# Kernel tuning notes

Hardware: AMD Instinct MI355X
Metric: run time of the kernel (lower is better)

The kernel has to match this reference:

```python
import jax, jax.numpy as jnp
import numpy as np

N = 50000   # nodes
E = 800000  # edges (avg degree 16)
IN, H, OUT = 128, 128, 64


def setup_inputs() -> dict:
    key = jax.random.key(0)
    ks = jax.random.split(key, 8)

    def w(k, shape):
        fan_in = shape[0]
        return (jax.random.normal(k, shape, jnp.float32) / np.float32(np.sqrt(fan_in)))

    x = jax.random.normal(ks[0], (N, IN), jnp.float32)
    edge_index = jax.random.randint(ks[1], (2, E), 0, N, jnp.int64)
    return {
        "x": x,
        "edge_index": edge_index,
        "W1": w(ks[2], (IN, H)), "b1": jnp.zeros((H,), jnp.float32),
        "W2": w(ks[3], (H, H)),  "b2": jnp.zeros((H,), jnp.float32),
        "W3": w(ks[4], (H, H)),  "b3": jnp.zeros((H,), jnp.float32),
        "Wd1": w(ks[5], (H, H)), "bd1": jnp.zeros((H,), jnp.float32),
        "Wd2": w(ks[6], (H, OUT)), "bd2": jnp.zeros((OUT,), jnp.float32),
    }


def _gcn_conv(x, src, dst, norm, W, b):
    # x: [N, Cin] -> linear transform, gather along edges, normalized scatter-add
    h = x @ W                                   # [N, Cout]
    msg = h[src] * norm[:, None]                # [E+N, Cout]
    out = jax.ops.segment_sum(msg, dst, num_segments=N)
    return out + b


def reference(x, edge_index, W1, b1, W2, b2, W3, b3, Wd1, bd1, Wd2, bd2):
    # Add self-loops (PyG GCNConv default) and compute symmetric normalization.
    loops = jnp.arange(N, dtype=edge_index.dtype)
    src = jnp.concatenate([edge_index[0], loops])   # [E+N]
    dst = jnp.concatenate([edge_index[1], loops])   # [E+N]
    deg = jax.ops.segment_sum(jnp.ones_like(dst, dtype=x.dtype), dst, num_segments=N)
    dinv = jnp.where(deg > 0, jax.lax.rsqrt(deg), jnp.zeros_like(deg))
    norm = dinv[src] * dinv[dst]                    # [E+N]

    h = jax.nn.relu(_gcn_conv(x, src, dst, norm, W1, b1))
    h = jax.nn.relu(_gcn_conv(h, src, dst, norm, W2, b2))
    h = jax.nn.relu(_gcn_conv(h, src, dst, norm, W3, b3))

    h = jax.nn.relu(h @ Wd1 + bd1)
    return jax.nn.sigmoid(h @ Wd2 + bd2)            # [N, OUT]
```

## Files before the change

### kernel.cpp

```cpp
#include <hip/hip_runtime.h>
#include <hip/hip_bf16.h>
#include <hip/hip_fp16.h>

#define N_NODES 50000
#define N_EDGES 800000
#define C_H 128
#define C_OUT 64
#define NBLK 196
#define TSTRIDE 136
#define E_PAD 950272
#define MM_BLKS 782
#define TILE_N 6250

typedef __attribute__((ext_vector_type(8))) short bf16x8;
typedef __attribute__((ext_vector_type(4))) float f32x4;

static __device__ __forceinline__ float bf_lo(unsigned int u) { return __uint_as_float(u << 16); }
static __device__ __forceinline__ float bf_hi(unsigned int u) { return __uint_as_float(u & 0xffff0000u); }
static __device__ __forceinline__ unsigned short f2bf(float f) {
    __hip_bfloat16 h = __float2bfloat16(f);
    return *(unsigned short*)&h;
}
static __device__ __forceinline__ unsigned int pack2(float a, float b) {
    return (unsigned int)f2bf(a) | ((unsigned int)f2bf(b) << 16);
}
static __device__ __forceinline__ unsigned short f2h_bits(float f) {
    union { __half h; unsigned short u; } c; c.h = __float2half_rn(f); return c.u;
}
static __device__ __forceinline__ float h_bits2f(unsigned short u) {
    union { __half h; unsigned short u; } c; c.u = u; return __half2float(c.h);
}

__global__ void prep_kernel(const int* __restrict__ src, const int* __restrict__ dst,
                            int* __restrict__ counts2,
                            int* __restrict__ rank,
                            const float* __restrict__ W1, const float* __restrict__ W2,
                            const float* __restrict__ W3, const float* __restrict__ Wd1,
                            const float* __restrict__ Wd2,
                            unsigned short* __restrict__ P1, unsigned short* __restrict__ P2,
                            unsigned short* __restrict__ P3, unsigned short* __restrict__ Pd1,
                            unsigned short* __restrict__ Pd2,
                            unsigned int* __restrict__ epay) {
    int b = blockIdx.x;
    if (b < 3125) {
        int e = b * 256 + threadIdx.x;
        int d = dst[e], s = src[e];
        int t = s / TILE_N;
        rank[e] = atomicAdd(&counts2[d * 8 + t], 1);
    } else if (b < 3413) {
        int idx = (b - 3125) * 256 + threadIdx.x;
        if (idx < 4 * 16384) {
            int which = idx >> 14;
            int r = idx & 16383;
            const float* W = (which == 0) ? W1 : (which == 1) ? W2 : (which == 2) ? W3 : Wd1;
            unsigned short* P = (which == 0) ? P1 : (which == 1) ? P2 : (which == 2) ? P3 : Pd1;
            int j = r & 7, lane = (r >> 3) & 63, t = r >> 9;
            int nb = t & 7, kb = t >> 3;
            int k = kb * 32 + ((lane >> 4) << 3) + j;
            int n = nb * 16 + (lane & 15);
            P[r] = f2bf(W[(size_t)k * 128 + n]);
        } else {
            int r = idx - 65536;
            if (r < 8192) {
                int j = r & 7, lane = (r >> 3) & 63, t = r >> 9;
                int nb = t & 3, kb = t >> 2;
                int k = kb * 32 + ((lane >> 4) << 3) + j;
                int n = nb * 16 + (lane & 15);
                Pd2[r] = f2bf(Wd2[(size_t)k * 64 + n]);
            }
        }
    } else {
        int i = (b - 3413) * 256 + threadIdx.x;
        *(uint4*)(epay + (size_t)i * 4) = make_uint4(0, 0, 0, 0);
    }
}

__global__ void __launch_bounds__(256) scan1_kernel(int* __restrict__ counts2,
                                                    int* __restrict__ eblk,
                                                    int* __restrict__ bsum,
                                                    float* __restrict__ dinv) {
    __shared__ int ws[4];
    int i = blockIdx.x * 256 + threadIdx.x;
    int deg = 0;
    if (i < N_NODES) {
        int* c = counts2 + (size_t)i * 8;
        uint4 a = *(uint4*)c;
        uint4 bq = *(uint4*)(c + 4);
        int run = 0, tv;
        tv = a.x;  a.x  = run; run += tv;
        tv = a.y;  a.y  = run; run += tv;
        tv = a.z;  a.z  = run; run += tv;
        tv = a.w;  a.w  = run; run += tv;
        tv = bq.x; bq.x = run; run += tv;
        tv = bq.y; bq.y = run; run += tv;
        tv = bq.z; bq.z = run; run += tv;
        tv = bq.w; bq.w = run; run += tv;
        deg = run;
        *(uint4*)c = a;
        *(uint4*)(c + 4) = bq;
        dinv[i] = rsqrtf((float)deg + 1.0f);
    }
    int vp = (deg + 3) & ~3;
    int lane = threadIdx.x & 63, w = threadIdx.x >> 6;
    int x = vp;
    #pragma unroll
    for (int off = 1; off < 64; off <<= 1) {
        int t = __shfl_up(x, off, 64);
        if (lane >= off) x += t;
    }
    if (lane == 63) ws[w] = x;
    __syncthreads();
    if (threadIdx.x == 0) {
        int run = 0;
        #pragma unroll
        for (int k = 0; k < 4; ++k) { int t = ws[k]; ws[k] = run; run += t; }
        bsum[blockIdx.x] = run;
    }
    __syncthreads();
    if (i < N_NODES) eblk[i] = x - vp + ws[w];
}

__global__ void __launch_bounds__(256) scanB_kernel(const int* __restrict__ eblk,
                                                    const int* __restrict__ bsum,
                                                    int* __restrict__ rowptr) {
    __shared__ int ws[4];
    __shared__ int sbo;
    int i = threadIdx.x;
    int v = (i < NBLK) ? bsum[i] : 0;
    int lane = i & 63, w = i >> 6;
    int x = v;
    #pragma unroll
    for (int off = 1; off < 64; off <<= 1) {
        int t = __shfl_up(x, off, 64);
        if (lane >= off) x += t;
    }
    if (lane == 63) ws[w] = x;
    __syncthreads();
    if (i == 0) {
        int run = 0;
        #pragma unroll
        for (int k = 0; k < 4; ++k) { int t = ws[k]; ws[k] = run; run += t; }
    }
    __syncthreads();
    int excl = x - v + ws[w];
    if (i == (int)blockIdx.x) sbo = excl;
    if (blockIdx.x == 0 && i == NBLK - 1) rowptr[N_NODES] = excl + v;
    __syncthreads();
    int g = blockIdx.x * 256 + threadIdx.x;
    if (g < N_NODES) rowptr[g] = eblk[g] + sbo;
}

__global__ void __launch_bounds__(256) fill_mm_kernel(
        const float* __restrict__ x, const unsigned short* __restrict__ P1,
        unsigned short* __restrict__ XW1,
        const int* __restrict__ src, const int* __restrict__ dst,
        const float* __restrict__ dinv,
        const int* __restrict__ rowptr, const int* __restrict__ counts2,
        const int* __restrict__ rank,
        unsigned int* __restrict__ epay) {
    int b = blockIdx.x;
    if (b < MM_BLKS) {
        const int lane = threadIdx.x & 63;
        const int wave = threadIdx.x >> 6;
        const int wid  = b * 4 + wave;
        if (wid * 16 >= N_NODES) return;
        const int node = wid * 16 + (lane & 15);
        const int quad = lane >> 4;
        f32x4 acc[8];
        #pragma unroll
        for (int nb = 0; nb < 8; ++nb) acc[nb] = (f32x4){0.f, 0.f, 0.f, 0.f};
        #pragma unroll
        for (int kb = 0; kb < 4; ++kb) {
            const float* p = x + (size_t)node * 128 + kb * 32 + quad * 8;
            float4 lo = *(const float4*)p;
            float4 hi = *(const float4*)(p + 4);
            union { bf16x8 v; unsigned int u[4]; } tmp;
            tmp.u[0] = pack2(lo.x, lo.y); tmp.u[1] = pack2(lo.z, lo.w);
            tmp.u[2] = pack2(hi.x, hi.y); tmp.u[3] = pack2(hi.z, hi.w);
            #pragma unroll
            for (int nb = 0; nb < 8; ++nb) {
                bf16x8 wf = *(const bf16x8*)(P1 + ((size_t)(kb * 8 + nb) * 64 + lane) * 8);
                acc[nb] = __builtin_amdgcn_mfma_f32_16x16x32_bf16(wf, tmp.v, acc[nb], 0, 0, 0);
            }
        }
        #pragma unroll
        for (int nb = 0; nb < 8; ++nb) {
            int ch = nb * 16 + quad * 4;
            uint2 o;
            o.x = pack2(acc[nb][0], acc[nb][1]);
            o.y = pack2(acc[nb][2], acc[nb][3]);
            *(uint2*)(XW1 + (size_t)node * C_H + ch) = o;
        }
    } else {
        int e = (b - MM_BLKS) * 256 + threadIdx.x;
        if (e < N_EDGES) {
            int d = dst[e], s = src[e];
            int t = s / TILE_N;
            int pos = rowptr[d] + counts2[d * 8 + t] + rank[e];
            float nrm = dinv[s] * dinv[d];
            epay[pos] = (unsigned int)s | ((unsigned int)f2h_bits(nrm) << 16);
        }
    }
}

__global__ void __launch_bounds__(256) gather1_kernel(
        const int* __restrict__ rowptr,
        const unsigned int* __restrict__ epay,
        const float* __restrict__ dinv,
        const unsigned short* __restrict__ hin,
        const float* __restrict__ bias,
        unsigned short* __restrict__ out) {
    int t    = blockIdx.x * 256 + threadIdx.x;
    int node = t >> 4;
    int c8   = (t & 15) << 3;

    float di = dinv[node], dii = di * di;
    uint4 raw = *(const uint4*)(hin + (size_t)node * C_H + c8);
    float a0 = bf_lo(raw.x) * dii, a1 = bf_hi(raw.x) * dii;
    float a2 = bf_lo(raw.y) * dii, a3 = bf_hi(raw.y) * dii;
    float a4 = bf_lo(raw.z) * dii, a5 = bf_hi(raw.z) * dii;
    float a6 = bf_lo(raw.w) * dii, a7 = bf_hi(raw.w) * dii;
    int beg = rowptr[node], end = rowptr[node + 1];
    int p = beg;
    for (; p + 8 <= end; p += 8) {
        uint4 ev0 = *(const uint4*)(epay + p);
        uint4 ev1 = *(const uint4*)(epay + p + 4);
        unsigned int ee[8] = {ev0.x, ev0.y, ev0.z, ev0.w, ev1.x, ev1.y, ev1.z, ev1.w};
        uint4 rv[8];
        #pragma unroll
        for (int j = 0; j < 8; ++j)
            rv[j] = *(const uint4*)(hin + (size_t)(ee[j] & 0xffffu) * C_H + c8);
        #pragma unroll
        for (int j = 0; j < 8; ++j) {
            float nm = h_bits2f((unsigned short)(ee[j] >> 16));
            a0 = fmaf(bf_lo(rv[j].x), nm, a0); a1 = fmaf(bf_hi(rv[j].x), nm, a1);
            a2 = fmaf(bf_lo(rv[j].y), nm, a2); a3 = fmaf(bf_hi(rv[j].y), nm, a3);
            a4 = fmaf(bf_lo(rv[j].z), nm, a4); a5 = fmaf(bf_hi(rv[j].z), nm, a5);
            a6 = fmaf(bf_lo(rv[j].w), nm, a6); a7 = fmaf(bf_hi(rv[j].w), nm, a7);
        }
    }
    if (p < end) {
        uint4 ev = *(const uint4*)(epay + p);
        unsigned int ee[4] = {ev.x, ev.y, ev.z, ev.w};
        uint4 rv[4];
        #pragma unroll
        for (int j = 0; j < 4; ++j)
            rv[j] = *(const uint4*)(hin + (size_t)(ee[j] & 0xffffu) * C_H + c8);
        #pragma unroll
        for (int j = 0; j < 4; ++j) {
            float nm = h_bits2f((unsigned short)(ee[j] >> 16));
            a0 = fmaf(bf_lo(rv[j].x), nm, a0); a1 = fmaf(bf_hi(rv[j].x), nm, a1);
            a2 = fmaf(bf_lo(rv[j].y), nm, a2); a3 = fmaf(bf_hi(rv[j].y), nm, a3);
            a4 = fmaf(bf_lo(rv[j].z), nm, a4); a5 = fmaf(bf_hi(rv[j].z), nm, a5);
            a6 = fmaf(bf_lo(rv[j].w), nm, a6); a7 = fmaf(bf_hi(rv[j].w), nm, a7);
        }
    }
    float4 ba = *(const float4*)(bias + c8);
    float4 bb = *(const float4*)(bias + c8 + 4);
    a0 = fmaxf(a0 + ba.x, 0.f); a1 = fmaxf(a1 + ba.y, 0.f);
    a2 = fmaxf(a2 + ba.z, 0.f); a3 = fmaxf(a3 + ba.w, 0.f);
    a4 = fmaxf(a4 + bb.x, 0.f); a5 = fmaxf(a5 + bb.y, 0.f);
    a6 = fmaxf(a6 + bb.z, 0.f); a7 = fmaxf(a7 + bb.w, 0.f);
    uint4 o;
    o.x = pack2(a0, a1); o.y = pack2(a2, a3);
    o.z = pack2(a4, a5); o.w = pack2(a6, a7);
    *(uint4*)(out + (size_t)node * C_H + c8) = o;
}

template <bool FINAL>
__global__ void __launch_bounds__(256) fused_layer_kernel(
        const int* __restrict__ rowptr,
        const unsigned int* __restrict__ epay,
        const float* __restrict__ dinv,
        const unsigned short* __restrict__ hin,
        const unsigned short* __restrict__ Wp,
        const float* __restrict__ bias,
        const unsigned short* __restrict__ Wd1p,
        const float* __restrict__ bd1,
        const unsigned short* __restrict__ Wd2p,
        const float* __restrict__ bd2,
        unsigned short* __restrict__ out_b,
        float* __restrict__ out_f) {
    __shared__ unsigned short sG[16 * TSTRIDE];
    const int t = threadIdx.x;

    {
        int nl = t >> 4, c8 = (t & 15) << 3;
        int node = blockIdx.x * 16 + nl;
        float di = dinv[node], dii = di * di;
        uint4 raw = *(const uint4*)(hin + (size_t)node * C_H + c8);
        float a0 = bf_lo(raw.x) * dii, a1 = bf_hi(raw.x) * dii;
        float a2 = bf_lo(raw.y) * dii, a3 = bf_hi(raw.y) * dii;
        float a4 = bf_lo(raw.z) * dii, a5 = bf_hi(raw.z) * dii;
        float a6 = bf_lo(raw.w) * dii, a7 = bf_hi(raw.w) * dii;
        int beg = rowptr[node], end = rowptr[node + 1];
        int p = beg;
        for (; p + 8 <= end; p += 8) {
            uint4 ev0 = *(const uint4*)(epay + p);
            uint4 ev1 = *(const uint4*)(epay + p + 4);
            unsigned int ee[8] = {ev0.x, ev0.y, ev0.z, ev0.w, ev1.x, ev1.y, ev1.z, ev1.w};
            uint4 rv[8];
            #pragma unroll
            for (int j = 0; j < 8; ++j)
                rv[j] = *(const uint4*)(hin + (size_t)(ee[j] & 0xffffu) * C_H + c8);
            #pragma unroll
            for (int j = 0; j < 8; ++j) {
                float nm = h_bits2f((unsigned short)(ee[j] >> 16));
                a0 = fmaf(bf_lo(rv[j].x), nm, a0); a1 = fmaf(bf_hi(rv[j].x), nm, a1);
                a2 = fmaf(bf_lo(rv[j].y), nm, a2); a3 = fmaf(bf_hi(rv[j].y), nm, a3);
                a4 = fmaf(bf_lo(rv[j].z), nm, a4); a5 = fmaf(bf_hi(rv[j].z), nm, a5);
                a6 = fmaf(bf_lo(rv[j].w), nm, a6); a7 = fmaf(bf_hi(rv[j].w), nm, a7);
            }
        }
        if (p < end) {
            uint4 ev = *(const uint4*)(epay + p);
            unsigned int ee[4] = {ev.x, ev.y, ev.z, ev.w};
            uint4 rv[4];
            #pragma unroll
            for (int j = 0; j < 4; ++j)
                rv[j] = *(const uint4*)(hin + (size_t)(ee[j] & 0xffffu) * C_H + c8);
            #pragma unroll
            for (int j = 0; j < 4; ++j) {
                float nm = h_bits2f((unsigned short)(ee[j] >> 16));
                a0 = fmaf(bf_lo(rv[j].x), nm, a0); a1 = fmaf(bf_hi(rv[j].x), nm, a1);
                a2 = fmaf(bf_lo(rv[j].y), nm, a2); a3 = fmaf(bf_hi(rv[j].y), nm, a3);
                a4 = fmaf(bf_lo(rv[j].z), nm, a4); a5 = fmaf(bf_hi(rv[j].z), nm, a5);
                a6 = fmaf(bf_lo(rv[j].w), nm, a6); a7 = fmaf(bf_hi(rv[j].w), nm, a7);
            }
        }
        uint4 o;
        o.x = pack2(a0, a1); o.y = pack2(a2, a3);
        o.z = pack2(a4, a5); o.w = pack2(a6, a7);
        *(uint4*)(sG + nl * TSTRIDE + c8) = o;
    }
    __syncthreads();

    const int lane = t & 63, wave = t >> 6, quad = lane >> 4, row = lane & 15;
    const int node = blockIdx.x * 16 + row;

    f32x4 acc0 = (f32x4){0.f, 0.f, 0.f, 0.f};
    f32x4 acc1 = (f32x4){0.f, 0.f, 0.f, 0.f};
    const int nb0 = 2 * wave, nb1 = 2 * wave + 1;
    #pragma unroll
    for (int kb = 0; kb < 4; ++kb) {
        bf16x8 hf = *(const bf16x8*)(sG + row * TSTRIDE + kb * 32 + quad * 8);
        bf16x8 wf0 = *(const bf16x8*)(Wp + ((size_t)(kb * 8 + nb0) * 64 + lane) * 8);
        bf16x8 wf1 = *(const bf16x8*)(Wp + ((size_t)(kb * 8 + nb1) * 64 + lane) * 8);
        acc0 = __builtin_amdgcn_mfma_f32_16x16x32_bf16(wf0, hf, acc0, 0, 0, 0);
        acc1 = __builtin_amdgcn_mfma_f32_16x16x32_bf16(wf1, hf, acc1, 0, 0, 0);
    }
    float4 ba0 = *(const float4*)(bias + nb0 * 16 + quad * 4);
    float4 ba1 = *(const float4*)(bias + nb1 * 16 + quad * 4);
    float v00 = fmaxf(acc0[0] + ba0.x, 0.f), v01 = fmaxf(acc0[1] + ba0.y, 0.f);
    float v02 = fmaxf(acc0[2] + ba0.z, 0.f), v03 = fmaxf(acc0[3] + ba0.w, 0.f);
    float v10 = fmaxf(acc1[0] + ba1.x, 0.f), v11 = fmaxf(acc1[1] + ba1.y, 0.f);
    float v12 = fmaxf(acc1[2] + ba1.z, 0.f), v13 = fmaxf(acc1[3] + ba1.w, 0.f);

    if (!FINAL) {
        uint2 o0, o1;
        o0.x = pack2(v00, v01); o0.y = pack2(v02, v03);
        o1.x = pack2(v10, v11); o1.y = pack2(v12, v13);
        *(uint2*)(out_b + (size_t)node * C_H + nb0 * 16 + quad * 4) = o0;
        *(uint2*)(out_b + (size_t)node * C_H + nb1 * 16 + quad * 4) = o1;
        return;
    }

    __syncthreads();
    {
        uint2 o0, o1;
        o0.x = pack2(v00, v01); o0.y = pack2(v02, v03);
        o1.x = pack2(v10, v11); o1.y = pack2(v12, v13);
        *(uint2*)(sG + row * TSTRIDE + nb0 * 16 + quad * 4) = o0;
        *(uint2*)(sG + row * TSTRIDE + nb1 * 16 + quad * 4) = o1;
    }
    __syncthreads();

    acc0 = (f32x4){0.f, 0.f, 0.f, 0.f};
    acc1 = (f32x4){0.f, 0.f, 0.f, 0.f};
    #pragma unroll
    for (int kb = 0; kb < 4; ++kb) {
        bf16x8 hf = *(const bf16x8*)(sG + row * TSTRIDE + kb * 32 + quad * 8);
        bf16x8 wf0 = *(const bf16x8*)(Wd1p + ((size_t)(kb * 8 + nb0) * 64 + lane) * 8);
        bf16x8 wf1 = *(const bf16x8*)(Wd1p + ((size_t)(kb * 8 + nb1) * 64 + lane) * 8);
        acc0 = __builtin_amdgcn_mfma_f32_16x16x32_bf16(wf0, hf, acc0, 0, 0, 0);
        acc1 = __builtin_amdgcn_mfma_f32_16x16x32_bf16(wf1, hf, acc1, 0, 0, 0);
    }
    ba0 = *(const float4*)(bd1 + nb0 * 16 + quad * 4);
    ba1 = *(const float4*)(bd1 + nb1 * 16 + quad * 4);
    v00 = fmaxf(acc0[0] + ba0.x, 0.f); v01 = fmaxf(acc0[1] + ba0.y, 0.f);
    v02 = fmaxf(acc0[2] + ba0.z, 0.f); v03 = fmaxf(acc0[3] + ba0.w, 0.f);
    v10 = fmaxf(acc1[0] + ba1.x, 0.f); v11 = fmaxf(acc1[1] + ba1.y, 0.f);
    v12 = fmaxf(acc1[2] + ba1.z, 0.f); v13 = fmaxf(acc1[3] + ba1.w, 0.f);
    __syncthreads();
    {
        uint2 o0, o1;
        o0.x = pack2(v00, v01); o0.y = pack2(v02, v03);
        o1.x = pack2(v10, v11); o1.y = pack2(v12, v13);
        *(uint2*)(sG + row * TSTRIDE + nb0 * 16 + quad * 4) = o0;
        *(uint2*)(sG + row * TSTRIDE + nb1 * 16 + quad * 4) = o1;
    }
    __syncthreads();

    f32x4 acc = (f32x4){0.f, 0.f, 0.f, 0.f};
    #pragma unroll
    for (int kb = 0; kb < 4; ++kb) {
        bf16x8 hf = *(const bf16x8*)(sG + row * TSTRIDE + kb * 32 + quad * 8);
        bf16x8 wf = *(const bf16x8*)(Wd2p + ((size_t)(kb * 4 + wave) * 64 + lane) * 8);
        acc = __builtin_amdgcn_mfma_f32_16x16x32_bf16(wf, hf, acc, 0, 0, 0);
    }
    int ch = wave * 16 + quad * 4;
    float4 b4 = *(const float4*)(bd2 + ch);
    float4 r;
    r.x = 1.f / (1.f + expf(-(acc[0] + b4.x)));
    r.y = 1.f / (1.f + expf(-(acc[1] + b4.y)));
    r.z = 1.f / (1.f + expf(-(acc[2] + b4.z)));
    r.w = 1.f / (1.f + expf(-(acc[3] + b4.w)));
    *(float4*)(out_f + (size_t)node * C_OUT + ch) = r;
}

extern "C" void kernel_launch(void* const* d_in, const int* in_sizes, int n_in,
                              void* d_out, int out_size, void* d_ws, size_t ws_size,
                              hipStream_t stream) {
    const float* x   = (const float*)d_in[0];
    const int*   ei  = (const int*)d_in[1];
    const float* W1  = (const float*)d_in[2];
    const float* b1  = (const float*)d_in[3];
    const float* W2  = (const float*)d_in[4];
    const float* b2  = (const float*)d_in[5];
    const float* W3  = (const float*)d_in[6];
    const float* b3  = (const float*)d_in[7];
    const float* Wd1 = (const float*)d_in[8];
    const float* bd1 = (const float*)d_in[9];
    const float* Wd2 = (const float*)d_in[10];
    const float* bd2 = (const float*)d_in[11];

    const int* src = ei;
    const int* dst = ei + N_EDGES;

    char* base = (char*)d_ws;
    size_t off = 0;
    auto alloc = [&](size_t bytes) { char* p = base + off; off += (bytes + 255) & ~size_t(255); return p; };
    int*            counts2 = (int*)alloc((size_t)N_NODES * 8 * 4);
    unsigned int*   epay   = (unsigned int*)alloc((size_t)E_PAD * 4);
    int*            rank   = (int*)alloc((size_t)N_EDGES * 4);
    float*          dinv   = (float*)alloc(N_NODES * 4);
    int*            rowptr = (int*)alloc((N_NODES + 1) * 4);
    int*            eblk   = (int*)alloc(N_NODES * 4);
    int*            bsum   = (int*)alloc(256 * 4);
    unsigned short* XW1    = (unsigned short*)alloc((size_t)N_NODES * C_H * 2);
    unsigned short* bufA   = (unsigned short*)alloc((size_t)N_NODES * C_H * 2);
    unsigned short* bufB   = (unsigned short*)alloc((size_t)N_NODES * C_H * 2);
    unsigned short* P1     = (unsigned short*)alloc(128 * 128 * 2);
    unsigned short* P2     = (unsigned short*)alloc(128 * 128 * 2);
    unsigned short* P3     = (unsigned short*)alloc(128 * 128 * 2);
    unsigned short* Pd1    = (unsigned short*)alloc(128 * 128 * 2);
    unsigned short* Pd2    = (unsigned short*)alloc(128 * 64 * 2);

    const int T = 256;
    dim3 blk(T);
    dim3 gN((N_NODES + T - 1) / T);
    dim3 gPrep(3125 + 288 + 928);
    dim3 gFillMM(MM_BLKS + 3125);
    dim3 gFused(N_NODES / 16);

    hipMemsetAsync(counts2, 0, (size_t)N_NODES * 8 * 4, stream);
    prep_kernel<<<gPrep, blk, 0, stream>>>(src, dst, counts2, rank,
                                           W1, W2, W3, Wd1, Wd2,
                                           P1, P2, P3, Pd1, Pd2, epay);
    scan1_kernel<<<gN, blk, 0, stream>>>(counts2, eblk, bsum, dinv);
    scanB_kernel<<<gN, blk, 0, stream>>>(eblk, bsum, rowptr);
    fill_mm_kernel<<<gFillMM, blk, 0, stream>>>(x, P1, XW1, src, dst, dinv,
                                                rowptr, counts2, rank, epay);

    gather1_kernel<<<gFused, blk, 0, stream>>>(rowptr, epay, dinv, XW1, b1, bufA);
    fused_layer_kernel<false><<<gFused, blk, 0, stream>>>(
        rowptr, epay, dinv, bufA, P2, b2, nullptr, nullptr, nullptr, nullptr, bufB, nullptr);
    fused_layer_kernel<true><<<gFused, blk, 0, stream>>>(
        rowptr, epay, dinv, bufB, P3, b3, Pd1, bd1, Pd2, bd2, nullptr, (float*)d_out);
}
```

Before: 252.7 us.

## Aggregate 64 nodes per block with 4 threads per node and per-tile pair padding

The gather and fused layer kernels now give each node 4 threads covering 32 channels each, and each block handles 64 nodes, with the MFMA stage looping over four 16-row tiles. Edge lists are now padded to even length per source tile rather than to multiples of 4 per node, and edges are processed in pairs walking the 8 source-tile segments. Both changes aim to cut wasted padded-edge work and to improve locality of the neighbour-row reads. The cost is 32 float accumulators per thread with a launch bound of 4 blocks, larger shared memory, and fewer threads per node, which may expose more memory latency.

```diff
diff --git a/kernel.cpp b/kernel.cpp
--- a/kernel.cpp
+++ b/kernel.cpp
@@ -8,9 +8,10 @@
 #define C_OUT 64
 #define NBLK 196
 #define TSTRIDE 136
-#define E_PAD 950272
+#define E_PAD 1200128
 #define MM_BLKS 782
 #define TILE_N 6250
+#define GB 782
 
 typedef __attribute__((ext_vector_type(8))) short bf16x8;
 typedef __attribute__((ext_vector_type(4))) float f32x4;
@@ -81,26 +82,26 @@
                                                     float* __restrict__ dinv) {
     __shared__ int ws[4];
     int i = blockIdx.x * 256 + threadIdx.x;
-    int deg = 0;
+    int vp = 0;
     if (i < N_NODES) {
         int* c = counts2 + (size_t)i * 8;
         uint4 a = *(uint4*)c;
         uint4 bq = *(uint4*)(c + 4);
+        int raw = a.x + a.y + a.z + a.w + bq.x + bq.y + bq.z + bq.w;
+        dinv[i] = rsqrtf((float)raw + 1.0f);
         int run = 0, tv;
-        tv = a.x;  a.x  = run; run += tv;
-        tv = a.y;  a.y  = run; run += tv;
-        tv = a.z;  a.z  = run; run += tv;
-        tv = a.w;  a.w  = run; run += tv;
-        tv = bq.x; bq.x = run; run += tv;
-        tv = bq.y; bq.y = run; run += tv;
-        tv = bq.z; bq.z = run; run += tv;
-        tv = bq.w; bq.w = run; run += tv;
-        deg = run;
+        tv = ((int)a.x + 1) & ~1;  a.x  = run; run += tv;
+        tv = ((int)a.y + 1) & ~1;  a.y  = run; run += tv;
+        tv = ((int)a.z + 1) & ~1;  a.z  = run; run += tv;
+        tv = ((int)a.w + 1) & ~1;  a.w  = run; run += tv;
+        tv = ((int)bq.x + 1) & ~1; bq.x = run; run += tv;
+        tv = ((int)bq.y + 1) & ~1; bq.y = run; run += tv;
+        tv = ((int)bq.z + 1) & ~1; bq.z = run; run += tv;
+        tv = ((int)bq.w + 1) & ~1; bq.w = run; run += tv;
+        vp = run;
         *(uint4*)c = a;
         *(uint4*)(c + 4) = bq;
-        dinv[i] = rsqrtf((float)deg + 1.0f);
-    }
-    int vp = (deg + 3) & ~3;
+    }
     int lane = threadIdx.x & 63, w = threadIdx.x >> 6;
     int x = vp;
     #pragma unroll
@@ -203,73 +204,88 @@
     }
 }
 
-__global__ void __launch_bounds__(256) gather1_kernel(
-        const int* __restrict__ rowptr,
+static __device__ __forceinline__ void fma8v(float* a, uint4 q, float nm) {
+    a[0] = fmaf(bf_lo(q.x), nm, a[0]); a[1] = fmaf(bf_hi(q.x), nm, a[1]);
+    a[2] = fmaf(bf_lo(q.y), nm, a[2]); a[3] = fmaf(bf_hi(q.y), nm, a[3]);
+    a[4] = fmaf(bf_lo(q.z), nm, a[4]); a[5] = fmaf(bf_hi(q.z), nm, a[5]);
+    a[6] = fmaf(bf_lo(q.w), nm, a[6]); a[7] = fmaf(bf_hi(q.w), nm, a[7]);
+}
+
+static __device__ __forceinline__ void agg32(
+        const int* __restrict__ rowptr, const int* __restrict__ counts2,
+        const unsigned int* __restrict__ epay,
+        const unsigned short* __restrict__ hin,
+        const float* __restrict__ dinv,
+        int node, int cb, float* acc) {
+    const unsigned short* hc = hin + cb;
+    float di = dinv[node], dii = di * di;
+    {
+        const unsigned short* rp = hc + (size_t)node * C_H;
+        uint4 q0 = *(const uint4*)rp,        q1 = *(const uint4*)(rp + 8);
+        uint4 q2 = *(const uint4*)(rp + 16), q3 = *(const uint4*)(rp + 24);
+        fma8v(acc + 0, q0, dii); fma8v(acc + 8, q1, dii);
+        fma8v(acc + 16, q2, dii); fma8v(acc + 24, q3, dii);
+    }
+    int base = rowptr[node];
+    int rend = rowptr[node + 1];
+    const int* boff = counts2 + (size_t)node * 8;
+    #pragma unroll 1
+    for (int t = 0; t < 8; ++t) {
+        int b0 = base + boff[t];
+        int b1 = (t == 7) ? rend : base + boff[t + 1];
+        for (int p = b0; p < b1; p += 2) {
+            uint2 ev = *(const uint2*)(epay + p);
+            const unsigned short* ra = hc + (size_t)(ev.x & 0xffffu) * C_H;
+            const unsigned short* rb = hc + (size_t)(ev.y & 0xffffu) * C_H;
+            uint4 a0 = *(const uint4*)ra,        a1 = *(const uint4*)(ra + 8);
+            uint4 a2 = *(const uint4*)(ra + 16), a3 = *(const uint4*)(ra + 24);
+            uint4 c0 = *(const uint4*)rb,        c1 = *(const uint4*)(rb + 8);
+            uint4 c2 = *(const uint4*)(rb + 16), c3 = *(const uint4*)(rb + 24);
+            float na = h_bits2f((unsigned short)(ev.x >> 16));
+            float nb = h_bits2f((unsigned short)(ev.y >> 16));
+            fma8v(acc + 0, a0, na); fma8v(acc + 8, a1, na);
+            fma8v(acc + 16, a2, na); fma8v(acc + 24, a3, na);
+            fma8v(acc + 0, c0, nb); fma8v(acc + 8, c1, nb);
+            fma8v(acc + 16, c2, nb); fma8v(acc + 24, c3, nb);
+        }
+    }
+}
+
+__global__ void __launch_bounds__(256, 4) gather1_kernel(
+        const int* __restrict__ rowptr, const int* __restrict__ counts2,
         const unsigned int* __restrict__ epay,
         const float* __restrict__ dinv,
         const unsigned short* __restrict__ hin,
         const float* __restrict__ bias,
         unsigned short* __restrict__ out) {
-    int t    = blockIdx.x * 256 + threadIdx.x;
-    int node = t >> 4;
-    int c8   = (t & 15) << 3;
-
-    float di = dinv[node], dii = di * di;
-    uint4 raw = *(const uint4*)(hin + (size_t)node * C_H + c8);
-    float a0 = bf_lo(raw.x) * dii, a1 = bf_hi(raw.x) * dii;
-    float a2 = bf_lo(raw.y) * dii, a3 = bf_hi(raw.y) * dii;
-    float a4 = bf_lo(raw.z) * dii, a5 = bf_hi(raw.z) * dii;
-    float a6 = bf_lo(raw.w) * dii, a7 = bf_hi(raw.w) * dii;
-    int beg = rowptr[node], end = rowptr[node + 1];
-    int p = beg;
-    for (; p + 8 <= end; p += 8) {
-        uint4 ev0 = *(const uint4*)(epay + p);
-        uint4 ev1 = *(const uint4*)(epay + p + 4);
-        unsigned int ee[8] = {ev0.x, ev0.y, ev0.z, ev0.w, ev1.x, ev1.y, ev1.z, ev1.w};
-        uint4 rv[8];
-        #pragma unroll
-        for (int j = 0; j < 8; ++j)
-            rv[j] = *(const uint4*)(hin + (size_t)(ee[j] & 0xffffu) * C_H + c8);
-        #pragma unroll
-        for (int j = 0; j < 8; ++j) {
-            float nm = h_bits2f((unsigned short)(ee[j] >> 16));
-            a0 = fmaf(bf_lo(rv[j].x), nm, a0); a1 = fmaf(bf_hi(rv[j].x), nm, a1);
-            a2 = fmaf(bf_lo(rv[j].y), nm, a2); a3 = fmaf(bf_hi(rv[j].y), nm, a3);
-            a4 = fmaf(bf_lo(rv[j].z), nm, a4); a5 = fmaf(bf_hi(rv[j].z), nm, a5);
-            a6 = fmaf(bf_lo(rv[j].w), nm, a6); a7 = fmaf(bf_hi(rv[j].w), nm, a7);
-        }
-    }
-    if (p < end) {
-        uint4 ev = *(const uint4*)(epay + p);
-        unsigned int ee[4] = {ev.x, ev.y, ev.z, ev.w};
-        uint4 rv[4];
-        #pragma unroll
-        for (int j = 0; j < 4; ++j)
-            rv[j] = *(const uint4*)(hin + (size_t)(ee[j] & 0xffffu) * C_H + c8);
-        #pragma unroll
-        for (int j = 0; j < 4; ++j) {
-            float nm = h_bits2f((unsigned short)(ee[j] >> 16));
-            a0 = fmaf(bf_lo(rv[j].x), nm, a0); a1 = fmaf(bf_hi(rv[j].x), nm, a1);
-            a2 = fmaf(bf_lo(rv[j].y), nm, a2); a3 = fmaf(bf_hi(rv[j].y), nm, a3);
-            a4 = fmaf(bf_lo(rv[j].z), nm, a4); a5 = fmaf(bf_hi(rv[j].z), nm, a5);
-            a6 = fmaf(bf_lo(rv[j].w), nm, a6); a7 = fmaf(bf_hi(rv[j].w), nm, a7);
-        }
-    }
-    float4 ba = *(const float4*)(bias + c8);
-    float4 bb = *(const float4*)(bias + c8 + 4);
-    a0 = fmaxf(a0 + ba.x, 0.f); a1 = fmaxf(a1 + ba.y, 0.f);
-    a2 = fmaxf(a2 + ba.z, 0.f); a3 = fmaxf(a3 + ba.w, 0.f);
-    a4 = fmaxf(a4 + bb.x, 0.f); a5 = fmaxf(a5 + bb.y, 0.f);
-    a6 = fmaxf(a6 + bb.z, 0.f); a7 = fmaxf(a7 + bb.w, 0.f);
-    uint4 o;
-    o.x = pack2(a0, a1); o.y = pack2(a2, a3);
-    o.z = pack2(a4, a5); o.w = pack2(a6, a7);
-    *(uint4*)(out + (size_t)node * C_H + c8) = o;
+    const int t = threadIdx.x;
+    const int node = blockIdx.x * 64 + (t >> 2);
+    if (node >= N_NODES) return;
+    const int cb = (t & 3) << 5;
+
+    float acc[32];
+    #pragma unroll
+    for (int j = 0; j < 32; ++j) acc[j] = 0.f;
+    agg32(rowptr, counts2, epay, hin, dinv, node, cb, acc);
+
+    #pragma unroll
+    for (int g = 0; g < 4; ++g) {
+        float4 ba = *(const float4*)(bias + cb + g * 8);
+        float4 bb = *(const float4*)(bias + cb + g * 8 + 4);
+        float v0 = fmaxf(acc[g*8+0] + ba.x, 0.f), v1 = fmaxf(acc[g*8+1] + ba.y, 0.f);
+        float v2 = fmaxf(acc[g*8+2] + ba.z, 0.f), v3 = fmaxf(acc[g*8+3] + ba.w, 0.f);
+        float v4 = fmaxf(acc[g*8+4] + bb.x, 0.f), v5 = fmaxf(acc[g*8+5] + bb.y, 0.f);
+        float v6 = fmaxf(acc[g*8+6] + bb.z, 0.f), v7 = fmaxf(acc[g*8+7] + bb.w, 0.f);
+        uint4 o;
+        o.x = pack2(v0, v1); o.y = pack2(v2, v3);
+        o.z = pack2(v4, v5); o.w = pack2(v6, v7);
+        *(uint4*)(out + (size_t)node * C_H + cb + g * 8) = o;
+    }
 }
 
 template <bool FINAL>
-__global__ void __launch_bounds__(256) fused_layer_kernel(
-        const int* __restrict__ rowptr,
+__global__ void __launch_bounds__(256, 4) fused_layer_kernel(
+        const int* __restrict__ rowptr, const int* __restrict__ counts2,
         const unsigned int* __restrict__ epay,
         const float* __restrict__ dinv,
         const unsigned short* __restrict__ hin,
@@ -281,141 +297,117 @@
         const float* __restrict__ bd2,
         unsigned short* __restrict__ out_b,
         float* __restrict__ out_f) {
-    __shared__ unsigned short sG[16 * TSTRIDE];
+    __shared__ unsigned short sA[64 * TSTRIDE];
+    __shared__ unsigned short sB[64 * TSTRIDE];
     const int t = threadIdx.x;
 
     {
-        int nl = t >> 4, c8 = (t & 15) << 3;
-        int node = blockIdx.x * 16 + nl;
-        float di = dinv[node], dii = di * di;
-        uint4 raw = *(const uint4*)(hin + (size_t)node * C_H + c8);
-        float a0 = bf_lo(raw.x) * dii, a1 = bf_hi(raw.x) * dii;
-        float a2 = bf_lo(raw.y) * dii, a3 = bf_hi(raw.y) * dii;
-        float a4 = bf_lo(raw.z) * dii, a5 = bf_hi(raw.z) * dii;
-        float a6 = bf_lo(raw.w) * dii, a7 = bf_hi(raw.w) * dii;
-        int beg = rowptr[node], end = rowptr[node + 1];
-        int p = beg;
-        for (; p + 8 <= end; p += 8) {
-            uint4 ev0 = *(const uint4*)(epay + p);
-            uint4 ev1 = *(const uint4*)(epay + p + 4);
-            unsigned int ee[8] = {ev0.x, ev0.y, ev0.z, ev0.w, ev1.x, ev1.y, ev1.z, ev1.w};
-            uint4 rv[8];
-            #pragma unroll
-            for (int j = 0; j < 8; ++j)
-                rv[j] = *(const uint4*)(hin + (size_t)(ee[j] & 0xffffu) * C_H + c8);
-            #pragma unroll
-            for (int j = 0; j < 8; ++j) {
-                float nm = h_bits2f((unsigned short)(ee[j] >> 16));
-                a0 = fmaf(bf_lo(rv[j].x), nm, a0); a1 = fmaf(bf_hi(rv[j].x), nm, a1);
-                a2 = fmaf(bf_lo(rv[j].y), nm, a2); a3 = fmaf(bf_hi(rv[j].y), nm, a3);
-                a4 = fmaf(bf_lo(rv[j].z), nm, a4); a5 = fmaf(bf_hi(rv[j].z), nm, a5);
-                a6 = fmaf(bf_lo(rv[j].w), nm, a6); a7 = fmaf(bf_hi(rv[j].w), nm, a7);
-            }
-        }
-        if (p < end) {
-            uint4 ev = *(const uint4*)(epay + p);
-            unsigned int ee[4] = {ev.x, ev.y, ev.z, ev.w};
-            uint4 rv[4];
-            #pragma unroll
-            for (int j = 0; j < 4; ++j)
-                rv[j] = *(const uint4*)(hin + (size_t)(ee[j] & 0xffffu) * C_H + c8);
-            #pragma unroll
-            for (int j = 0; j < 4; ++j) {
-                float nm = h_bits2f((unsigned short)(ee[j] >> 16));
-                a0 = fmaf(bf_lo(rv[j].x), nm, a0); a1 = fmaf(bf_hi(rv[j].x), nm, a1);
-                a2 = fmaf(bf_lo(rv[j].y), nm, a2); a3 = fmaf(bf_hi(rv[j].y), nm, a3);
-                a4 = fmaf(bf_lo(rv[j].z), nm, a4); a5 = fmaf(bf_hi(rv[j].z), nm, a5);
-                a6 = fmaf(bf_lo(rv[j].w), nm, a6); a7 = fmaf(bf_hi(rv[j].w), nm, a7);
-            }
-        }
-        uint4 o;
-        o.x = pack2(a0, a1); o.y = pack2(a2, a3);
-        o.z = pack2(a4, a5); o.w = pack2(a6, a7);
-        *(uint4*)(sG + nl * TSTRIDE + c8) = o;
+        const int ln = t >> 2;
+        const int node = blockIdx.x * 64 + ln;
+        const int cb = (t & 3) << 5;
+        float acc[32];
+        #pragma unroll
+        for (int j = 0; j < 32; ++j) acc[j] = 0.f;
+        if (node < N_NODES)
+            agg32(rowptr, counts2, epay, hin, dinv, node, cb, acc);
+        #pragma unroll
+        for (int g = 0; g < 4; ++g) {
+            uint4 o;
+            o.x = pack2(acc[g*8+0], acc[g*8+1]); o.y = pack2(acc[g*8+2], acc[g*8+3]);
+            o.z = pack2(acc[g*8+4], acc[g*8+5]); o.w = pack2(acc[g*8+6], acc[g*8+7]);
+            *(uint4*)(sA + ln * TSTRIDE + cb + g * 8) = o;
+        }
     }
     __syncthreads();
 
     const int lane = t & 63, wave = t >> 6, quad = lane >> 4, row = lane & 15;
-    const int node = blockIdx.x * 16 + row;
-
-    f32x4 acc0 = (f32x4){0.f, 0.f, 0.f, 0.f};
-    f32x4 acc1 = (f32x4){0.f, 0.f, 0.f, 0.f};
     const int nb0 = 2 * wave, nb1 = 2 * wave + 1;
-    #pragma unroll
-    for (int kb = 0; kb < 4; ++kb) {
-        bf16x8 hf = *(const bf16x8*)(sG + row * TSTRIDE + kb * 32 + quad * 8);
-        bf16x8 wf0 = *(const bf16x8*)(Wp + ((size_t)(kb * 8 + nb0) * 64 + lane) * 8);
-        bf16x8 wf1 = *(const bf16x8*)(Wp + ((size_t)(kb * 8 + nb1) * 64 + lane) * 8);
-        acc0 = __builtin_amdgcn_mfma_f32_16x16x32_bf16(wf0, hf, acc0, 0, 0, 0);
-        acc1 = __builtin_amdgcn_mfma_f32_16x16x32_bf16(wf1, hf, acc1, 0, 0, 0);
-    }
-    float4 ba0 = *(const float4*)(bias + nb0 * 16 + quad * 4);
-    float4 ba1 = *(const float4*)(bias + nb1 * 16 + quad * 4);
-    float v00 = fmaxf(acc0[0] + ba0.x, 0.f), v01 = fmaxf(acc0[1] + ba0.y, 0.f);
-    float v02 = fmaxf(acc0[2] + ba0.z, 0.f), v03 = fmaxf(acc0[3] + ba0.w, 0.f);
-    float v10 = fmaxf(acc1[0] + ba1.x, 0.f), v11 = fmaxf(acc1[1] + ba1.y, 0.f);
-    float v12 = fmaxf(acc1[2] + ba1.z, 0.f), v13 = fmaxf(acc1[3] + ba1.w, 0.f);
-
-    if (!FINAL) {
+
+    #pragma unroll 1
+    for (int rt = 0; rt < 4; ++rt) {
+        const int lrow = rt * 16 + row;
+        const int node = blockIdx.x * 64 + lrow;
+        f32x4 acc0 = (f32x4){0.f, 0.f, 0.f, 0.f};
+        f32x4 acc1 = (f32x4){0.f, 0.f, 0.f, 0.f};
+        #pragma unroll
+        for (int kb = 0; kb < 4; ++kb) {
+            bf16x8 hf = *(const bf16x8*)(sA + lrow * TSTRIDE + kb * 32 + quad * 8);
+            bf16x8 wf0 = *(const bf16x8*)(Wp + ((size_t)(kb * 8 + nb0) * 64 + lane) * 8);
+            bf16x8 wf1 = *(const bf16x8*)(Wp + ((size_t)(kb * 8 + nb1) * 64 + lane) * 8);
+            acc0 = __builtin_amdgcn_mfma_f32_16x16x32_bf16(wf0, hf, acc0, 0, 0, 0);
+            acc1 = __builtin_amdgcn_mfma_f32_16x16x32_bf16(wf1, hf, acc1, 0, 0, 0);
+        }
+        float4 ba0 = *(const float4*)(bias + nb0 * 16 + quad * 4);
+        float4 ba1 = *(const float4*)(bias + nb1 * 16 + quad * 4);
+        float v00 = fmaxf(acc0[0] + ba0.x, 0.f), v01 = fmaxf(acc0[1] + ba0.y, 0.f);
+        float v02 = fmaxf(acc0[2] + ba0.z, 0.f), v03 = fmaxf(acc0[3] + ba0.w, 0.f);
+        float v10 = fmaxf(acc1[0] + ba1.x, 0.f), v11 = fmaxf(acc1[1] + ba1.y, 0.f);
+        float v12 = fmaxf(acc1[2] + ba1.z, 0.f), v13 = fmaxf(acc1[3] + ba1.w, 0.f);
         uint2 o0, o1;
         o0.x = pack2(v00, v01); o0.y = pack2(v02, v03);
         o1.x = pack2(v10, v11); o1.y = pack2(v12, v13);
-        *(uint2*)(out_b + (size_t)node * C_H + nb0 * 16 + quad * 4) = o0;
-        *(uint2*)(out_b + (size_t)node * C_H + nb1 * 16 + quad * 4) = o1;
-        return;
-    }
-
-    __syncthreads();
-    {
+        if (!FINAL) {
+            if (node < N_NODES) {
+                *(uint2*)(out_b + (size_t)node * C_H + nb0 * 16 + quad * 4) = o0;
+                *(uint2*)(out_b + (size_t)node * C_H + nb1 * 16 + quad * 4) = o1;
+            }
+        } else {
+            *(uint2*)(sB + lrow * TSTRIDE + nb0 * 16 + quad * 4) = o0;
+            *(uint2*)(sB + lrow * TSTRIDE + nb1 * 16 + quad * 4) = o1;
+        }
+    }
+    if (!FINAL) return;
+
+    __syncthreads();
+    #pragma unroll 1
+    for (int rt = 0; rt < 4; ++rt) {
+        const int lrow = rt * 16 + row;
+        f32x4 acc0 = (f32x4){0.f, 0.f, 0.f, 0.f};
+        f32x4 acc1 = (f32x4){0.f, 0.f, 0.f, 0.f};
+        #pragma unroll
+        for (int kb = 0; kb < 4; ++kb) {
+            bf16x8 hf = *(const bf16x8*)(sB + lrow * TSTRIDE + kb * 32 + quad * 8);
+            bf16x8 wf0 = *(const bf16x8*)(Wd1p + ((size_t)(kb * 8 + nb0) * 64 + lane) * 8);
+            bf16x8 wf1 = *(const bf16x8*)(Wd1p + ((size_t)(kb * 8 + nb1) * 64 + lane) * 8);
+            acc0 = __builtin_amdgcn_mfma_f32_16x16x32_bf16(wf0, hf, acc0, 0, 0, 0);
+            acc1 = __builtin_amdgcn_mfma_f32_16x16x32_bf16(wf1, hf, acc1, 0, 0, 0);
+        }
+        float4 ba0 = *(const float4*)(bd1 + nb0 * 16 + quad * 4);
+        float4 ba1 = *(const float4*)(bd1 + nb1 * 16 + quad * 4);
+        float v00 = fmaxf(acc0[0] + ba0.x, 0.f), v01 = fmaxf(acc0[1] + ba0.y, 0.f);
+        float v02 = fmaxf(acc0[2] + ba0.z, 0.f), v03 = fmaxf(acc0[3] + ba0.w, 0.f);
+        float v10 = fmaxf(acc1[0] + ba1.x, 0.f), v11 = fmaxf(acc1[1] + ba1.y, 0.f);
+        float v12 = fmaxf(acc1[2] + ba1.z, 0.f), v13 = fmaxf(acc1[3] + ba1.w, 0.f);
         uint2 o0, o1;
         o0.x = pack2(v00, v01); o0.y = pack2(v02, v03);
         o1.x = pack2(v10, v11); o1.y = pack2(v12, v13);
-        *(uint2*)(sG + row * TSTRIDE + nb0 * 16 + quad * 4) = o0;
-        *(uint2*)(sG + row * TSTRIDE + nb1 * 16 + quad * 4) = o1;
-    }
-    __syncthreads();
-
-    acc0 = (f32x4){0.f, 0.f, 0.f, 0.f};
-    acc1 = (f32x4){0.f, 0.f, 0.f, 0.f};
-    #pragma unroll
-    for (int kb = 0; kb < 4; ++kb) {
-        bf16x8 hf = *(const bf16x8*)(sG + row * TSTRIDE + kb * 32 + quad * 8);
-        bf16x8 wf0 = *(const bf16x8*)(Wd1p + ((size_t)(kb * 8 + nb0) * 64 + lane) * 8);
-        bf16x8 wf1 = *(const bf16x8*)(Wd1p + ((size_t)(kb * 8 + nb1) * 64 + lane) * 8);
-        acc0 = __builtin_amdgcn_mfma_f32_16x16x32_bf16(wf0, hf, acc0, 0, 0, 0);
-        acc1 = __builtin_amdgcn_mfma_f32_16x16x32_bf16(wf1, hf, acc1, 0, 0, 0);
-    }
-    ba0 = *(const float4*)(bd1 + nb0 * 16 + quad * 4);
-    ba1 = *(const float4*)(bd1 + nb1 * 16 + quad * 4);
-    v00 = fmaxf(acc0[0] + ba0.x, 0.f); v01 = fmaxf(acc0[1] + ba0.y, 0.f);
-    v02 = fmaxf(acc0[2] + ba0.z, 0.f); v03 = fmaxf(acc0[3] + ba0.w, 0.f);
-    v10 = fmaxf(acc1[0] + ba1.x, 0.f); v11 = fmaxf(acc1[1] + ba1.y, 0.f);
-    v12 = fmaxf(acc1[2] + ba1.z, 0.f); v13 = fmaxf(acc1[3] + ba1.w, 0.f);
-    __syncthreads();
-    {
-        uint2 o0, o1;
-        o0.x = pack2(v00, v01); o0.y = pack2(v02, v03);
-        o1.x = pack2(v10, v11); o1.y = pack2(v12, v13);
-        *(uint2*)(sG + row * TSTRIDE + nb0 * 16 + quad * 4) = o0;
-        *(uint2*)(sG + row * TSTRIDE + nb1 * 16 + quad * 4) = o1;
-    }
-    __syncthreads();
-
-    f32x4 acc = (f32x4){0.f, 0.f, 0.f, 0.f};
-    #pragma unroll
-    for (int kb = 0; kb < 4; ++kb) {
-        bf16x8 hf = *(const bf16x8*)(sG + row * TSTRIDE + kb * 32 + quad * 8);
-        bf16x8 wf = *(const bf16x8*)(Wd2p + ((size_t)(kb * 4 + wave) * 64 + lane) * 8);
-        acc = __builtin_amdgcn_mfma_f32_16x16x32_bf16(wf, hf, acc, 0, 0, 0);
-    }
-    int ch = wave * 16 + quad * 4;
-    float4 b4 = *(const float4*)(bd2 + ch);
-    float4 r;
-    r.x = 1.f / (1.f + expf(-(acc[0] + b4.x)));
-    r.y = 1.f / (1.f + expf(-(acc[1] + b4.y)));
-    r.z = 1.f / (1.f + expf(-(acc[2] + b4.z)));
-    r.w = 1.f / (1.f + expf(-(acc[3] + b4.w)));
-    *(float4*)(out_f + (size_t)node * C_OUT + ch) = r;
+        *(uint2*)(sA + lrow * TSTRIDE + nb0 * 16 + quad * 4) = o0;
+        *(uint2*)(sA + lrow * TSTRIDE + nb1 * 16 + quad * 4) = o1;
+    }
+    __syncthreads();
+
+    #pragma unroll 1
+    for (int rt = 0; rt < 4; ++rt) {
+        const int lrow = rt * 16 + row;
+        const int node = blockIdx.x * 64 + lrow;
+        f32x4 acc = (f32x4){0.f, 0.f, 0.f, 0.f};
+        #pragma unroll
+        for (int kb = 0; kb < 4; ++kb) {
+            bf16x8 hf = *(const bf16x8*)(sA + lrow * TSTRIDE + kb * 32 + quad * 8);
+            bf16x8 wf = *(const bf16x8*)(Wd2p + ((size_t)(kb * 4 + wave) * 64 + lane) * 8);
+            acc = __builtin_amdgcn_mfma_f32_16x16x32_bf16(wf, hf, acc, 0, 0, 0);
+        }
+        if (node < N_NODES) {
+            int ch = wave * 16 + quad * 4;
+            float4 b4 = *(const float4*)(bd2 + ch);
+            float4 rr;
+            rr.x = 1.f / (1.f + expf(-(acc[0] + b4.x)));
+            rr.y = 1.f / (1.f + expf(-(acc[1] + b4.y)));
+            rr.z = 1.f / (1.f + expf(-(acc[2] + b4.z)));
+            rr.w = 1.f / (1.f + expf(-(acc[3] + b4.w)));
+            *(float4*)(out_f + (size_t)node * C_OUT + ch) = rr;
+        }
+    }
 }
 
 extern "C" void kernel_launch(void* const* d_in, const int* in_sizes, int n_in,
@@ -459,9 +451,9 @@
     const int T = 256;
     dim3 blk(T);
     dim3 gN((N_NODES + T - 1) / T);
-    dim3 gPrep(3125 + 288 + 928);
+    dim3 gPrep(3125 + 288 + 1172);
     dim3 gFillMM(MM_BLKS + 3125);
-    dim3 gFused(N_NODES / 16);
+    dim3 gGB(GB);
 
     hipMemsetAsync(counts2, 0, (size_t)N_NODES * 8 * 4, stream);
     prep_kernel<<<gPrep, blk, 0, stream>>>(src, dst, counts2, rank,
@@ -472,9 +464,9 @@
     fill_mm_kernel<<<gFillMM, blk, 0, stream>>>(x, P1, XW1, src, dst, dinv,
                                                 rowptr, counts2, rank, epay);
 
-    gather1_kernel<<<gFused, blk, 0, stream>>>(rowptr, epay, dinv, XW1, b1, bufA);
-    fused_layer_kernel<false><<<gFused, blk, 0, stream>>>(
-        rowptr, epay, dinv, bufA, P2, b2, nullptr, nullptr, nullptr, nullptr, bufB, nullptr);
-    fused_layer_kernel<true><<<gFused, blk, 0, stream>>>(
-        rowptr, epay, dinv, bufB, P3, b3, Pd1, bd1, Pd2, bd2, nullptr, (float*)d_out);
-}
+    gather1_kernel<<<gGB, blk, 0, stream>>>(rowptr, counts2, epay, dinv, XW1, b1, bufA);
+    fused_layer_kernel<false><<<gGB, blk, 0, stream>>>(
+        rowptr, counts2, epay, dinv, bufA, P2, b2, nullptr, nullptr, nullptr, nullptr, bufB, nullptr);
+    fused_layer_kernel<true><<<gGB, blk, 0, stream>>>(
+        rowptr, counts2, epay, dinv, bufB, P3, b3, Pd1, bd1, Pd2, bd2, nullptr, (float*)d_out);
+}
```

After: 293.9 us. 1.16x slower.
